# Optimization experiments

Hardware: AMD Instinct MI355X
Metric: run time of the kernel (lower is better)

Reference implementation:

```python
import jax, jax.numpy as jnp
import numpy as np

B, T, HW = 2, 16, 224
S = 14            # patch size after stem: 56 // 4
FEAT = 64 * S * S # 12544 per stream


def _stem(x, w):
    # I3D truncated at MaxPool3d_2a_3x3: Conv3d 7x7x7 stride 2 (+ReLU) then MaxPool (1,3,3) stride (1,2,2)
    y = jax.lax.conv_general_dilated(x, w, window_strides=(2, 2, 2), padding='SAME',
                                     dimension_numbers=('NCDHW', 'OIDHW', 'NCDHW'))
    y = jax.nn.relu(y)
    y = jax.lax.reduce_window(y, -jnp.inf, jax.lax.max,
                              (1, 1, 1, 3, 3), (1, 1, 1, 2, 2), 'SAME')
    return y  # [B,64,8,56,56]


def _fold_and_flatten(x):
    # torch: x.unfold(3,s,s).unfold(4,s,s).permute(0,2,3,4,1,5,6).flatten(4)
    b, c, t, h, w = x.shape
    x = x.reshape(b, c, t, h // S, S, w // S, S)          # (B,C,T,hb,hi,wb,wi)
    x = x.transpose(0, 2, 3, 5, 1, 4, 6)                  # (B,T,hb,wb,C,hi,wi)
    return x.reshape(b, t, h // S, w // S, c * S * S)      # (B,8,4,4,12544)


def _fcl(fr, ff, W1, b1, W2, b2, W3, b3):
    # vectorized over (B,T,H,W); dropout inactive (eval)
    x = jnp.concatenate([fr, ff], axis=-1)                 # (B,8,4,4,25088)
    x = jax.nn.relu(jnp.einsum('bthwf,fk->bthwk', x, W1) + b1)
    x = jax.nn.relu(jnp.einsum('bthwf,fk->bthwk', x, W2) + b2)
    return jax.nn.sigmoid(jnp.einsum('bthwf,fk->bthwk', x, W3) + b3)  # (B,8,4,4,1)


def _get_mask(rgbs, flows, w_rgb, w_flow, W1, b1, W2, b2, W3, b3):
    fr = _fold_and_flatten(_stem(rgbs, w_rgb))
    ff = _fold_and_flatten(_stem(flows, w_flow))
    m = _fcl(fr, ff, W1, b1, W2, b2, W3, b3)[..., 0]       # (B,T=8,H=4,W=4)
    m = jax.image.resize(m[:, None], (m.shape[0], 1, T, HW, HW), method='trilinear')
    return m[:, 0]                                          # (B,16,224,224)


def _masking(rgbs, mask, bg):
    # rgbs*mask + bg*(1-mask), broadcast over channel dim
    return rgbs * mask[:, None] + bg[None, :, None] * (1.0 - mask[:, None])


def _feature_head(x, w_feat, Wl, bl):
    # stand-in for full frozen I3D feature backbone: stem + global pool + linear logits
    y = _stem(x, w_feat)                                    # (B,64,8,56,56)
    pooled = y.mean(axis=(2, 3, 4))                         # (B,64)
    return pooled @ Wl + bl                                 # (B,400)


def setup_inputs() -> dict:
    key = jax.random.key(0)
    ks = jax.random.split(key, 10)
    n = lambda k, s, sc=1.0: jax.random.normal(k, s, dtype=jnp.float32) * sc
    return {
        'rgbs': n(ks[0], (B, 3, T, HW, HW)),
        'flows': n(ks[1], (B, 2, T, HW, HW)),
        'img_background': n(ks[2], (3, HW, HW)),
        'w_rgb': n(ks[3], (64, 3, 7, 7, 7), 0.05),
        'w_flow': n(ks[4], (64, 2, 7, 7, 7), 0.05),
        'w_feat': n(ks[5], (64, 3, 7, 7, 7), 0.05),
        'W1': n(ks[6], (2 * FEAT, 1024), 0.01), 'b1': jnp.zeros((1024,), jnp.float32),
        'W2': n(ks[7], (1024, 256), 0.03), 'b2': jnp.zeros((256,), jnp.float32),
        'W3': n(ks[8], (256, 1), 0.06), 'b3': jnp.zeros((1,), jnp.float32),
        'Wl': n(ks[9], (64, 400), 0.1), 'bl': jnp.zeros((400,), jnp.float32),
    }


def reference(rgbs, flows, img_background, w_rgb, w_flow, w_feat,
              W1, b1, W2, b2, W3, b3, Wl, bl):
    mask = _get_mask(rgbs, flows, w_rgb, w_flow, W1, b1, W2, b2, W3, b3)
    masked0 = _masking(rgbs, mask, img_background)
    masked1 = _masking(rgbs, 1.0 - mask, img_background)
    out0 = _feature_head(masked0, w_feat, Wl, bl)
    out1 = _feature_head(masked1, w_feat, Wl, bl)
    return out0, out1, mask
```

## Files before the change

### kernel.cpp

```cpp
#include <hip/hip_runtime.h>
#include <hip/hip_bf16.h>
#include <math.h>

#define IHW 224
#define DIN 16
#define DOUT 8
#define HO 112
#define PO 56
#define DP 21
#define HP 232
#define WP 240
#define PLANE (HP * WP)

typedef __bf16 bf16x8 __attribute__((ext_vector_type(8)));
typedef float f32x4 __attribute__((ext_vector_type(4)));
typedef float f32x16 __attribute__((ext_vector_type(16)));
typedef ushort u16x8 __attribute__((ext_vector_type(8)));

__device__ __forceinline__ ushort f2bf(float f) {
  uint u = __float_as_uint(f);
  uint r = (u + 0x7FFFu + ((u >> 16) & 1u)) >> 16;
  return (ushort)r;
}
__device__ __forceinline__ float bf2f(ushort u) {
  return __uint_as_float(((uint)u) << 16);
}

__global__ void cvt_pad(const float* __restrict__ in, ushort* __restrict__ out, int nbc) {
  const int v = blockIdx.x * 256 + threadIdx.x;
  const int total = nbc * DP * HP * (WP / 2);
  if (v >= total) return;
  const int pw2 = v % (WP / 2);
  int rest = v / (WP / 2);
  const int pih = rest % HP; rest /= HP;
  const int pid = rest % DP;
  const int bc = rest / DP;
  const int id = pid - 2, ih = pih - 2;
  ushort2 o = make_ushort2(0, 0);
  if (id >= 0 && id < DIN && ih >= 0 && ih < IHW) {
    const float* src = in + ((size_t)(bc * DIN + id) * IHW + ih) * IHW;
    const int iw0 = pw2 * 2 - 2;
    if (iw0 >= 0 && iw0 < IHW) o.x = f2bf(src[iw0]);
    if (iw0 + 1 >= 0 && iw0 + 1 < IHW) o.y = f2bf(src[iw0 + 1]);
  }
  reinterpret_cast<ushort2*>(out)[v] = o;
}

__global__ void masking_pad(const float* __restrict__ rgbs, const float* __restrict__ mask,
                            const float* __restrict__ bg, ushort* __restrict__ out) {
  const int v = blockIdx.x * 256 + threadIdx.x;
  const int total = 12 * DP * HP * (WP / 2);
  if (v >= total) return;
  const int pw2 = v % (WP / 2);
  int rest = v / (WP / 2);
  const int pih = rest % HP; rest /= HP;
  const int pid = rest % DP;
  const int bc = rest / DP;
  const int head = bc / 6;
  const int r6 = bc - head * 6;
  const int b = r6 / 3, c = r6 - (r6 / 3) * 3;
  const int t = pid - 2, ih = pih - 2;
  ushort2 o = make_ushort2(0, 0);
  if (t >= 0 && t < DIN && ih >= 0 && ih < IHW) {
    const float* mrow = mask + ((size_t)(b * DIN + t)) * (IHW * IHW) + ih * IHW;
    const float* rrow = rgbs + ((size_t)((b * 3 + c) * DIN + t)) * (IHW * IHW) + ih * IHW;
    const float* brow = bg + (size_t)c * (IHW * IHW) + ih * IHW;
    const int iw0 = pw2 * 2 - 2;
#pragma unroll
    for (int j = 0; j < 2; j++) {
      const int iw = iw0 + j;
      if (iw >= 0 && iw < IHW) {
        float m = mrow[iw];
        if (head) m = 1.f - m;
        const float val = rrow[iw] * m + brow[iw] * (1.f - m);
        if (j == 0) o.x = f2bf(val); else o.y = f2bf(val);
      }
    }
  }
  reinterpret_cast<ushort2*>(out)[v] = o;
}

template<int C>
__global__ __launch_bounds__(256) void wprep(const float* __restrict__ w, ushort* __restrict__ wB) {
  constexpr int C7 = C * 7, KREAL = C * 49, KPAD = (C == 3) ? 160 : 128;
  const int idx = blockIdx.x * 256 + threadIdx.x;
  if (idx >= 64 * 7 * KPAD) return;
  const int k = idx % KPAD;
  const int rest = idx / KPAD;
  const int kw = rest % 7;
  const int oc = rest / 7;
  float val = 0.f;
  if (k < KREAL) {
    const int kd = k / C7, rem = k % C7, c = rem / 7, kh = rem % 7;
    val = w[(((oc * C + c) * 7 + kd) * 7 + kh) * 7 + kw];
  }
  wB[idx] = f2bf(val);
}

template<int C>
__global__ __launch_bounds__(256, 4) void conv_mfma(
    const ushort* __restrict__ in, const ushort* __restrict__ wB,
    ushort* __restrict__ out)
{
  constexpr int C7 = C * 7, KREAL = C * 49;
  constexpr int KPAD = (C == 3) ? 160 : 128;
  constexpr int NKS = KPAD / 16;
  constexpr int ROWB = KPAD * 2;
  constexpr int KG = KPAD / 4;
  constexpr int SROWS = 118;
  constexpr int NU2 = KG * 64 / 256;
  constexpr int BAT = NU2 / 2;

  __shared__ char smem[SROWS * ROWB];
  __shared__ int offt[KPAD];

  const int bx = blockIdx.x;
  const int hx = (bx & 7) * 28 + (bx >> 3);
  const int ho = hx >> 1, half = hx & 1;
  const int dd = blockIdx.y;
  const int bb = blockIdx.z;
  const int tid = threadIdx.x;
  const int lane = tid & 63;
  const int wv = tid >> 6;

  if (tid < KPAD) {
    const int k = (tid < KREAL) ? tid : (KREAL - 1);
    const int kd = k / C7, rem = k % C7, c = rem / 7, kh = rem % 7;
    offt[tid] = ((bb * C + c) * DP + 2 * dd + kd) * PLANE + (2 * ho + kh) * WP;
  }
  __syncthreads();

  const int piwbase = half * 112;
  for (int itb = 0; itb < 2; itb++) {
    uint v4[BAT][4];
    int sbl[BAT], sbh[BAT];
#pragma unroll
    for (int i = 0; i < BAT; i++) {
      const int id = (itb * BAT + i) * 256 + tid;
      const int kg = id >> 6, sp = id & 63;
      const int s = sp * 2;
      const bool ok = (s < SROWS);
      const int piw = piwbase + s;
      const int4 ot = *reinterpret_cast<const int4*>(&offt[kg * 4]);
      v4[i][0] = *reinterpret_cast<const uint*>(in + (size_t)(ot.x + piw));
      v4[i][1] = *reinterpret_cast<const uint*>(in + (size_t)(ot.y + piw));
      v4[i][2] = *reinterpret_cast<const uint*>(in + (size_t)(ot.z + piw));
      v4[i][3] = *reinterpret_cast<const uint*>(in + (size_t)(ot.w + piw));
      const int m = (sp & 7) << 4;
      sbl[i] = ok ? ((s * ROWB + kg * 8) ^ m) : -1;
      sbh[i] = ok ? (((s + 1) * ROWB + kg * 8) ^ m) : -1;
    }
#pragma unroll
    for (int i = 0; i < BAT; i++) {
      if (sbl[i] >= 0) {
        ushort4 lo, hi;
        lo.x = (ushort)v4[i][0]; hi.x = (ushort)(v4[i][0] >> 16);
        lo.y = (ushort)v4[i][1]; hi.y = (ushort)(v4[i][1] >> 16);
        lo.z = (ushort)v4[i][2]; hi.z = (ushort)(v4[i][2] >> 16);
        lo.w = (ushort)v4[i][3]; hi.w = (ushort)(v4[i][3] >> 16);
        *reinterpret_cast<ushort4*>(smem + sbl[i]) = lo;
        *reinterpret_cast<ushort4*>(smem + sbh[i]) = hi;
      }
    }
  }
  __syncthreads();

  const int nh = wv & 1, kseg = wv >> 1;
  const int l31 = lane & 31, khf = lane >> 5;

  int sbase[2];
#pragma unroll
  for (int mt = 0; mt < 2; mt++) {
    int wo_l = mt * 32 + l31;
    if (wo_l > 55) wo_l = 55;
    sbase[mt] = 2 * wo_l;
  }
  const ushort* wq = wB + (size_t)(nh * 32 + l31) * (7 * KPAD) + khf * 8;

  f32x16 acc[2] = {};

  if (kseg == 0) {
#pragma unroll
    for (int kw = 0; kw < 4; kw++) {
      bf16x8 bq[NKS];
#pragma unroll
      for (int ks = 0; ks < NKS; ks++)
        bq[ks] = *reinterpret_cast<const bf16x8*>(wq + kw * KPAD + ks * 16);
#pragma unroll
      for (int ks = 0; ks < NKS; ks++) {
#pragma unroll
        for (int mt = 0; mt < 2; mt++) {
          const int s = sbase[mt] + kw;
          const int byte = (s * ROWB + ks * 32 + khf * 16) ^ (((s >> 1) & 7) << 4);
          const bf16x8 a = *reinterpret_cast<const bf16x8*>(smem + byte);
          acc[mt] = __builtin_amdgcn_mfma_f32_32x32x16_bf16(a, bq[ks], acc[mt], 0, 0, 0);
        }
      }
    }
  } else {
#pragma unroll
    for (int kw = 4; kw < 7; kw++) {
      bf16x8 bq[NKS];
#pragma unroll
      for (int ks = 0; ks < NKS; ks++)
        bq[ks] = *reinterpret_cast<const bf16x8*>(wq + kw * KPAD + ks * 16);
#pragma unroll
      for (int ks = 0; ks < NKS; ks++) {
#pragma unroll
        for (int mt = 0; mt < 2; mt++) {
          const int s = sbase[mt] + kw;
          const int byte = (s * ROWB + ks * 32 + khf * 16) ^ (((s >> 1) & 7) << 4);
          const bf16x8 a = *reinterpret_cast<const bf16x8*>(smem + byte);
          acc[mt] = __builtin_amdgcn_mfma_f32_32x32x16_bf16(a, bq[ks], acc[mt], 0, 0, 0);
        }
      }
    }
  }

  __syncthreads();
  float* redf = reinterpret_cast<float*>(smem);
  if (kseg == 1) {
#pragma unroll
    for (int mt = 0; mt < 2; mt++)
#pragma unroll
      for (int r = 0; r < 16; r++)
        redf[((nh * 2 + mt) * 16 + r) * 64 + lane] = acc[mt][r];
  }
  __syncthreads();
  if (kseg == 0) {
#pragma unroll
    for (int mt = 0; mt < 2; mt++)
#pragma unroll
      for (int r = 0; r < 16; r++)
        acc[mt][r] += redf[((nh * 2 + mt) * 16 + r) * 64 + lane];
  }
  __syncthreads();

  ushort* eLDS = reinterpret_cast<ushort*>(smem);
  if (kseg == 0) {
    const int oc = nh * 32 + l31;
#pragma unroll
    for (int mt = 0; mt < 2; mt++) {
#pragma unroll
      for (int q = 0; q < 4; q++) {
        const int wo_b = mt * 32 + q * 8 + khf * 4;
        if (wo_b < 56) {
          ushort4 r4;
          r4.x = f2bf(fmaxf(acc[mt][q * 4 + 0], 0.f));
          r4.y = f2bf(fmaxf(acc[mt][q * 4 + 1], 0.f));
          r4.z = f2bf(fmaxf(acc[mt][q * 4 + 2], 0.f));
          r4.w = f2bf(fmaxf(acc[mt][q * 4 + 3], 0.f));
          *reinterpret_cast<ushort4*>(eLDS + oc * 60 + wo_b) = r4;
        }
      }
    }
  }
  __syncthreads();
  ushort* gout = out + ((size_t)(bb * 64) * DOUT + dd) * (HO * HO) + ho * HO + half * 56;
#pragma unroll
  for (int i = 0; i < 4; i++) {
    const int idx = i * 256 + tid;
    if (idx < 896) {
      const int o2 = idx / 14;
      const int w4 = idx - o2 * 14;
      *reinterpret_cast<ushort4*>(gout + (size_t)o2 * DOUT * (HO * HO) + w4 * 4) =
          *reinterpret_cast<const ushort4*>(eLDS + o2 * 60 + w4 * 4);
    }
  }
}

__global__ void maxpool_gather(const ushort* __restrict__ in, ushort* __restrict__ X, int fbase) {
  const int idx = blockIdx.x * 256 + threadIdx.x;
  if (idx >= 2 * 64 * 8 * PO * 28) return;
  const int wo2 = idx % 28;
  const int ho = (idx / 28) % PO;
  const int rest = idx / (28 * PO);
  const ushort* p = in + (size_t)rest * (HO * HO);
  const int iwb = wo2 * 4;
  ushort m0 = 0, m1 = 0;
  for (int dh = 0; dh < 3; dh++) {
    const int ih = 2 * ho + dh;
    if (ih >= HO) break;
    const ushort* row = p + ih * HO;
    const ushort2 u0 = *reinterpret_cast<const ushort2*>(row + iwb);
    const ushort2 u1 = *reinterpret_cast<const ushort2*>(row + iwb + 2);
    const ushort e4 = (iwb + 4 < HO) ? row[iwb + 4] : (ushort)0;
    ushort a = (u0.x > u0.y) ? u0.x : u0.y;  a = (a > u1.x) ? a : u1.x;
    ushort b2 = (u1.x > u1.y) ? u1.x : u1.y; b2 = (b2 > e4) ? b2 : e4;
    m0 = (a > m0) ? a : m0;
    m1 = (b2 > m1) ? b2 : m1;
  }
  const int wo = wo2 * 2;
  const int t = rest % 8;
  const int c = (rest / 8) % 64;
  const int b = rest / 512;
  const int r = ((b * 8 + t) * 4 + ho / 14) * 4 + (wo / 14);
  const int f = fbase + c * 196 + (ho % 14) * 14 + (wo % 14);
  *reinterpret_cast<ushort2*>(X + (size_t)r * 25088 + f) = make_ushort2(m0, m1);
}

__global__ __launch_bounds__(512) void fcl1_mfma(
    const ushort* __restrict__ X, const float* __restrict__ W1, ushort* __restrict__ part)
{
  const int bn = blockIdx.x;
  const int kc = blockIdx.y;
  const int tid = threadIdx.x;
  const int lane = tid & 63;
  const int wv = tid >> 6;
  const int wm = wv >> 1, wn = wv & 1;
  const int l31 = lane & 31, kh = lane >> 5;

  __shared__ char xs[256 * 128];
  __shared__ char wsm[128 * 128];

  f32x16 acc[2][2] = {};

  const int kchunk0 = kc * 256;

  for (int kt = 0; kt < 4; kt++) {
    const int k0 = kchunk0 + kt * 64;
    __syncthreads();
#pragma unroll
    for (int i = 0; i < 4; i++) {
      const int chunk = tid + 512 * i;
      const int r = chunk >> 3, c8 = chunk & 7;
      const int4 v = *reinterpret_cast<const int4*>(X + (size_t)r * 25088 + k0 + c8 * 8);
      int byte = r * 128 + c8 * 16;
      byte ^= ((r & 7) << 4);
      *reinterpret_cast<int4*>(xs + byte) = v;
    }
    {
      const int nq = tid & 31, kp0 = tid >> 5;
#pragma unroll
      for (int h = 0; h < 2; h++) {
        const int kk = (kp0 + h * 16) * 2;
        const float4 a  = *reinterpret_cast<const float4*>(W1 + (size_t)(k0 + kk) * 1024 + bn * 128 + nq * 4);
        const float4 bq = *reinterpret_cast<const float4*>(W1 + (size_t)(k0 + kk + 1) * 1024 + bn * 128 + nq * 4);
        const float av[4] = {a.x, a.y, a.z, a.w};
        const float bv[4] = {bq.x, bq.y, bq.z, bq.w};
#pragma unroll
        for (int j = 0; j < 4; j++) {
          const int n = nq * 4 + j;
          const uint pack = (uint)f2bf(av[j]) | ((uint)f2bf(bv[j]) << 16);
          const int byte = (n * 128 + kk * 2) ^ ((n & 7) << 4);
          *reinterpret_cast<uint*>(wsm + byte) = pack;
        }
      }
    }
    __syncthreads();
#pragma unroll
    for (int ks = 0; ks < 4; ks++) {
      bf16x8 af[2], bfr[2];
#pragma unroll
      for (int m = 0; m < 2; m++) {
        const int r = wm * 64 + m * 32 + l31;
        const int byte = (r * 128 + ks * 32 + kh * 16) ^ ((r & 7) << 4);
        af[m] = *reinterpret_cast<const bf16x8*>(xs + byte);
      }
#pragma unroll
      for (int n = 0; n < 2; n++) {
        const int c = wn * 64 + n * 32 + l31;
        const int byte = (c * 128 + ks * 32 + kh * 16) ^ ((c & 7) << 4);
        bfr[n] = *reinterpret_cast<const bf16x8*>(wsm + byte);
      }
#pragma unroll
      for (int m = 0; m < 2; m++)
#pragma unroll
        for (int n = 0; n < 2; n++)
          acc[m][n] = __builtin_amdgcn_mfma_f32_32x32x16_bf16(af[m], bfr[n], acc[m][n], 0, 0, 0);
    }
  }

  ushort* pout = part + (size_t)kc * (256 * 1024);
#pragma unroll
  for (int m = 0; m < 2; m++)
#pragma unroll
    for (int n = 0; n < 2; n++)
#pragma unroll
      for (int rg = 0; rg < 16; rg++) {
        const int row = wm * 64 + m * 32 + (rg & 3) + 8 * (rg >> 2) + 4 * kh;
        const int col = bn * 128 + wn * 64 + n * 32 + l31;
        pout[(size_t)row * 1024 + col] = f2bf(acc[m][n][rg]);
      }
}

__global__ void h1_reduce(const ushort* __restrict__ part, const float* __restrict__ b1,
                          float* __restrict__ h1) {
  const int v = blockIdx.x * 256 + threadIdx.x;
  if (v >= 32768) return;
  const int r = v >> 7, n8 = v & 127;
  float s[8];
#pragma unroll
  for (int j = 0; j < 8; j++) s[j] = b1[n8 * 8 + j];
  for (int kc = 0; kc < 98; kc++) {
    const u16x8 p = *reinterpret_cast<const u16x8*>(part + (size_t)kc * 262144 + r * 1024 + n8 * 8);
#pragma unroll
    for (int j = 0; j < 8; j++) s[j] += bf2f(p[j]);
  }
#pragma unroll
  for (int j = 0; j < 8; j++) h1[r * 1024 + n8 * 8 + j] = fmaxf(s[j], 0.f);
}

__global__ __launch_bounds__(256) void fcl2_k(const float* __restrict__ h1,
                                              const float* __restrict__ W2,
                                              const float* __restrict__ b2,
                                              float* __restrict__ h2) {
  const int r0 = blockIdx.x * 4;
  const int n = threadIdx.x;
  __shared__ float xr[4][1024];
  for (int i = threadIdx.x; i < 4096; i += 256) xr[i >> 10][i & 1023] = h1[r0 * 1024 + i];
  __syncthreads();
  float acc[4] = {b2[n], b2[n], b2[n], b2[n]};
  for (int k = 0; k < 1024; k++) {
    const float w = W2[k * 256 + n];
#pragma unroll
    for (int r = 0; r < 4; r++) acc[r] += xr[r][k] * w;
  }
#pragma unroll
  for (int r = 0; r < 4; r++) h2[(r0 + r) * 256 + n] = fmaxf(acc[r], 0.f);
}

__global__ void fcl3_k(const float* __restrict__ h2, const float* __restrict__ W3,
                       const float* __restrict__ b3, float* __restrict__ ms) {
  __shared__ float w[256];
  w[threadIdx.x] = W3[threadIdx.x];
  __syncthreads();
  const int r = threadIdx.x;
  float s = b3[0];
  for (int k = 0; k < 256; k++) s += h2[r * 256 + k] * w[k];
  ms[r] = 1.f / (1.f + expf(-s));
}

__global__ void upsample_k(const float* __restrict__ ms, float* __restrict__ mask) {
  const int idx = blockIdx.x * 256 + threadIdx.x;
  if (idx >= 2 * 16 * IHW * IHW) return;
  const int w = idx % IHW;
  const int h = (idx / IHW) % IHW;
  const int t = (idx / (IHW * IHW)) % 16;
  const int b = idx / (16 * IHW * IHW);

  const float tf = t * 0.5f - 0.25f;
  const float hf = (h + 0.5f) * (1.f / 56.f) - 0.5f;
  const float wf = (w + 0.5f) * (1.f / 56.f) - 0.5f;

  int t0 = (int)floorf(tf); const float ft = tf - t0;
  int h0 = (int)floorf(hf); const float fh = hf - h0;
  int w0 = (int)floorf(wf); const float fw = wf - w0;
  const int t1 = min(t0 + 1, 7); t0 = max(t0, 0);
  const int h1 = min(h0 + 1, 3); h0 = max(h0, 0);
  const int w1 = min(w0 + 1, 3); w0 = max(w0, 0);

  const float* p = ms + b * 128;
  auto at = [&](int tt, int hh, int ww) { return p[(tt * 4 + hh) * 4 + ww]; };
  const float c00 = at(t0, h0, w0) * (1.f - fw) + at(t0, h0, w1) * fw;
  const float c01 = at(t0, h1, w0) * (1.f - fw) + at(t0, h1, w1) * fw;
  const float c10 = at(t1, h0, w0) * (1.f - fw) + at(t1, h0, w1) * fw;
  const float c11 = at(t1, h1, w0) * (1.f - fw) + at(t1, h1, w1) * fw;
  const float c0 = c00 * (1.f - fh) + c01 * fh;
  const float c1 = c10 * (1.f - fh) + c11 * fh;
  mask[idx] = c0 * (1.f - ft) + c1 * ft;
}

__global__ __launch_bounds__(256) void pool_sum_k(const ushort* __restrict__ in,
                                                  float* __restrict__ psums) {
  const int blk = blockIdx.x;
  const ushort* p = in + (size_t)blk * (HO * HO);
  float s = 0.f;
  for (int idx = threadIdx.x; idx < PO * PO; idx += 256) {
    const int ho = idx / PO, wo = idx % PO;
    ushort m = 0;
    for (int dh = 0; dh < 3; dh++) {
      const int ih = 2 * ho + dh;
      if (ih >= HO) break;
      for (int dw = 0; dw < 3; dw++) {
        const int iw = 2 * wo + dw;
        if (iw >= HO) break;
        const ushort v = p[ih * HO + iw];
        m = (v > m) ? v : m;
      }
    }
    s += bf2f(m);
  }
  __shared__ float red[256];
  red[threadIdx.x] = s;
  __syncthreads();
  for (int off = 128; off > 0; off >>= 1) {
    if (threadIdx.x < off) red[threadIdx.x] += red[threadIdx.x + off];
    __syncthreads();
  }
  if (threadIdx.x == 0) psums[blk] = red[0];
}

__global__ void logits_k(const float* __restrict__ psums, const float* __restrict__ Wl,
                         const float* __restrict__ bl, float* __restrict__ out) {
  const int idx = blockIdx.x * 256 + threadIdx.x;
  if (idx >= 1600) return;
  const int bf = idx / 400, l = idx % 400;
  float s = bl[l];
  for (int oc = 0; oc < 64; oc++) {
    float ps = 0.f;
    for (int t = 0; t < 8; t++) ps += psums[(bf * 64 + oc) * 8 + t];
    s += (ps * (1.f / 25088.f)) * Wl[oc * 400 + l];
  }
  out[idx] = s;
}

extern "C" void kernel_launch(void* const* d_in, const int* in_sizes, int n_in,
                              void* d_out, int out_size, void* d_ws, size_t ws_size,
                              hipStream_t stream) {
  const float* rgbs   = (const float*)d_in[0];
  const float* flows  = (const float*)d_in[1];
  const float* bg     = (const float*)d_in[2];
  const float* w_rgb  = (const float*)d_in[3];
  const float* w_flow = (const float*)d_in[4];
  const float* w_feat = (const float*)d_in[5];
  const float* W1     = (const float*)d_in[6];
  const float* b1     = (const float*)d_in[7];
  const float* W2     = (const float*)d_in[8];
  const float* b2     = (const float*)d_in[9];
  const float* W3     = (const float*)d_in[10];
  const float* b3     = (const float*)d_in[11];
  const float* Wl     = (const float*)d_in[12];
  const float* bl     = (const float*)d_in[13];
  float* out = (float*)d_out;

  float* ws = (float*)d_ws;
  ushort* convbuf = (ushort*)ws;
  ushort* part    = (ushort*)ws;
  ushort* X       = (ushort*)(ws + 12845056);
  ushort* rgbsP   = (ushort*)(ws + 16056320);
  ushort* flowsP  = (ushort*)(ws + 19564160);
  ushort* maskedP = (ushort*)(ws + 16056320);
  float*  h1      = ws + 23100000;
  float*  h2      = h1 + 262144;
  float*  msmall  = h2 + 65536;
  float*  psums   = msmall + 256;
  ushort* wrgb_b  = (ushort*)(psums + 2048);
  ushort* wflow_b = wrgb_b + 86016;
  ushort* wfeat_b = wflow_b + 57344;

  float* mask_full = out + 1600;

  cvt_pad<<<(3507840 + 255) / 256, 256, 0, stream>>>(rgbs, rgbsP, 6);
  cvt_pad<<<(2338560 + 255) / 256, 256, 0, stream>>>(flows, flowsP, 4);
  wprep<3><<<(64 * 7 * 160 + 255) / 256, 256, 0, stream>>>(w_rgb, wrgb_b);
  wprep<2><<<(64 * 7 * 128 + 255) / 256, 256, 0, stream>>>(w_flow, wflow_b);
  wprep<3><<<(64 * 7 * 160 + 255) / 256, 256, 0, stream>>>(w_feat, wfeat_b);

  conv_mfma<3><<<dim3(224, 8, 2), 256, 0, stream>>>(rgbsP, wrgb_b, convbuf);
  maxpool_gather<<<(1605632 + 255) / 256, 256, 0, stream>>>(convbuf, X, 0);
  conv_mfma<2><<<dim3(224, 8, 2), 256, 0, stream>>>(flowsP, wflow_b, convbuf);
  maxpool_gather<<<(1605632 + 255) / 256, 256, 0, stream>>>(convbuf, X, 12544);

  fcl1_mfma<<<dim3(8, 98), 512, 0, stream>>>(X, W1, part);
  h1_reduce<<<128, 256, 0, stream>>>(part, b1, h1);
  fcl2_k<<<64, 256, 0, stream>>>(h1, W2, b2, h2);
  fcl3_k<<<1, 256, 0, stream>>>(h2, W3, b3, msmall);
  upsample_k<<<(1605632 + 255) / 256, 256, 0, stream>>>(msmall, mask_full);

  masking_pad<<<(7015680 + 255) / 256, 256, 0, stream>>>(rgbs, mask_full, bg, maskedP);
  conv_mfma<3><<<dim3(224, 8, 4), 256, 0, stream>>>(maskedP, wfeat_b, convbuf);
  pool_sum_k<<<2048, 256, 0, stream>>>(convbuf, psums);
  logits_k<<<7, 256, 0, stream>>>(psums, Wl, bl, out);
}
```

Measured before the change: 449.6 us.

## Split conv K-loop across four wave groups with 512-thread blocks

Doubles conv_mfma block size to 512 threads so the seven kernel-width taps are split across four wave groups instead of two. Partial accumulators are combined through a two-level LDS reduction tree, and the staging and store loops are rescaled to the larger block. This shortens each wave's serial MFMA chain and raises wave count, at the cost of extra reduction barriers and uneven tap split. For the 2-channel variant the second reduction buffer may extend past the shared staging array.

```diff
diff --git a/kernel.cpp b/kernel.cpp
--- a/kernel.cpp
+++ b/kernel.cpp
@@ -98,7 +98,7 @@
 }
 
 template<int C>
-__global__ __launch_bounds__(256, 4) void conv_mfma(
+__global__ __launch_bounds__(512, 4) void conv_mfma(
     const ushort* __restrict__ in, const ushort* __restrict__ wB,
     ushort* __restrict__ out)
 {
@@ -108,8 +108,7 @@
   constexpr int ROWB = KPAD * 2;
   constexpr int KG = KPAD / 4;
   constexpr int SROWS = 118;
-  constexpr int NU2 = KG * 64 / 256;
-  constexpr int BAT = NU2 / 2;
+  constexpr int NU2 = KG * 64 / 512;
 
   __shared__ char smem[SROWS * ROWB];
   __shared__ int offt[KPAD];
@@ -130,13 +129,13 @@
   }
   __syncthreads();
 
-  const int piwbase = half * 112;
-  for (int itb = 0; itb < 2; itb++) {
-    uint v4[BAT][4];
-    int sbl[BAT], sbh[BAT];
-#pragma unroll
-    for (int i = 0; i < BAT; i++) {
-      const int id = (itb * BAT + i) * 256 + tid;
+  {
+    const int piwbase = half * 112;
+    uint v4[NU2][4];
+    int sbl[NU2], sbh[NU2];
+#pragma unroll
+    for (int i = 0; i < NU2; i++) {
+      const int id = i * 512 + tid;
       const int kg = id >> 6, sp = id & 63;
       const int s = sp * 2;
       const bool ok = (s < SROWS);
@@ -151,7 +150,7 @@
       sbh[i] = ok ? (((s + 1) * ROWB + kg * 8) ^ m) : -1;
     }
 #pragma unroll
-    for (int i = 0; i < BAT; i++) {
+    for (int i = 0; i < NU2; i++) {
       if (sbl[i] >= 0) {
         ushort4 lo, hi;
         lo.x = (ushort)v4[i][0]; hi.x = (ushort)(v4[i][0] >> 16);
@@ -179,52 +178,61 @@
 
   f32x16 acc[2] = {};
 
+  const int kwbeg = kseg * 2;
+  const int kwend = (kseg == 3) ? 7 : (kwbeg + 2);
+  for (int kw = kwbeg; kw < kwend; kw++) {
+#pragma unroll
+    for (int ks = 0; ks < NKS; ks++) {
+      const bf16x8 b = *reinterpret_cast<const bf16x8*>(wq + kw * KPAD + ks * 16);
+#pragma unroll
+      for (int mt = 0; mt < 2; mt++) {
+        const int s = sbase[mt] + kw;
+        const int byte = (s * ROWB + ks * 32 + khf * 16) ^ (((s >> 1) & 7) << 4);
+        const bf16x8 a = *reinterpret_cast<const bf16x8*>(smem + byte);
+        acc[mt] = __builtin_amdgcn_mfma_f32_32x32x16_bf16(a, b, acc[mt], 0, 0, 0);
+      }
+    }
+  }
+
+  __syncthreads();
+  float* buf0 = reinterpret_cast<float*>(smem);
+  float* buf1 = reinterpret_cast<float*>(smem + 16384);
+  if (kseg == 1) {
+#pragma unroll
+    for (int mt = 0; mt < 2; mt++)
+#pragma unroll
+      for (int r = 0; r < 16; r++)
+        buf0[((nh * 2 + mt) * 16 + r) * 64 + lane] = acc[mt][r];
+  }
+  if (kseg == 3) {
+#pragma unroll
+    for (int mt = 0; mt < 2; mt++)
+#pragma unroll
+      for (int r = 0; r < 16; r++)
+        buf1[((nh * 2 + mt) * 16 + r) * 64 + lane] = acc[mt][r];
+  }
+  __syncthreads();
   if (kseg == 0) {
 #pragma unroll
-    for (int kw = 0; kw < 4; kw++) {
-      bf16x8 bq[NKS];
-#pragma unroll
-      for (int ks = 0; ks < NKS; ks++)
-        bq[ks] = *reinterpret_cast<const bf16x8*>(wq + kw * KPAD + ks * 16);
-#pragma unroll
-      for (int ks = 0; ks < NKS; ks++) {
-#pragma unroll
-        for (int mt = 0; mt < 2; mt++) {
-          const int s = sbase[mt] + kw;
-          const int byte = (s * ROWB + ks * 32 + khf * 16) ^ (((s >> 1) & 7) << 4);
-          const bf16x8 a = *reinterpret_cast<const bf16x8*>(smem + byte);
-          acc[mt] = __builtin_amdgcn_mfma_f32_32x32x16_bf16(a, bq[ks], acc[mt], 0, 0, 0);
-        }
-      }
-    }
-  } else {
-#pragma unroll
-    for (int kw = 4; kw < 7; kw++) {
-      bf16x8 bq[NKS];
-#pragma unroll
-      for (int ks = 0; ks < NKS; ks++)
-        bq[ks] = *reinterpret_cast<const bf16x8*>(wq + kw * KPAD + ks * 16);
-#pragma unroll
-      for (int ks = 0; ks < NKS; ks++) {
-#pragma unroll
-        for (int mt = 0; mt < 2; mt++) {
-          const int s = sbase[mt] + kw;
-          const int byte = (s * ROWB + ks * 32 + khf * 16) ^ (((s >> 1) & 7) << 4);
-          const bf16x8 a = *reinterpret_cast<const bf16x8*>(smem + byte);
-          acc[mt] = __builtin_amdgcn_mfma_f32_32x32x16_bf16(a, bq[ks], acc[mt], 0, 0, 0);
-        }
-      }
-    }
-  }
-
-  __syncthreads();
-  float* redf = reinterpret_cast<float*>(smem);
-  if (kseg == 1) {
-#pragma unroll
     for (int mt = 0; mt < 2; mt++)
 #pragma unroll
       for (int r = 0; r < 16; r++)
-        redf[((nh * 2 + mt) * 16 + r) * 64 + lane] = acc[mt][r];
+        acc[mt][r] += buf0[((nh * 2 + mt) * 16 + r) * 64 + lane];
+  }
+  if (kseg == 2) {
+#pragma unroll
+    for (int mt = 0; mt < 2; mt++)
+#pragma unroll
+      for (int r = 0; r < 16; r++)
+        acc[mt][r] += buf1[((nh * 2 + mt) * 16 + r) * 64 + lane];
+  }
+  __syncthreads();
+  if (kseg == 2) {
+#pragma unroll
+    for (int mt = 0; mt < 2; mt++)
+#pragma unroll
+      for (int r = 0; r < 16; r++)
+        buf0[((nh * 2 + mt) * 16 + r) * 64 + lane] = acc[mt][r];
   }
   __syncthreads();
   if (kseg == 0) {
@@ -232,7 +240,7 @@
     for (int mt = 0; mt < 2; mt++)
 #pragma unroll
       for (int r = 0; r < 16; r++)
-        acc[mt][r] += redf[((nh * 2 + mt) * 16 + r) * 64 + lane];
+        acc[mt][r] += buf0[((nh * 2 + mt) * 16 + r) * 64 + lane];
   }
   __syncthreads();
 
@@ -258,8 +266,8 @@
   __syncthreads();
   ushort* gout = out + ((size_t)(bb * 64) * DOUT + dd) * (HO * HO) + ho * HO + half * 56;
 #pragma unroll
-  for (int i = 0; i < 4; i++) {
-    const int idx = i * 256 + tid;
+  for (int i = 0; i < 2; i++) {
+    const int idx = i * 512 + tid;
     if (idx < 896) {
       const int o2 = idx / 14;
       const int w4 = idx - o2 * 14;
@@ -547,9 +555,9 @@
   wprep<2><<<(64 * 7 * 128 + 255) / 256, 256, 0, stream>>>(w_flow, wflow_b);
   wprep<3><<<(64 * 7 * 160 + 255) / 256, 256, 0, stream>>>(w_feat, wfeat_b);
 
-  conv_mfma<3><<<dim3(224, 8, 2), 256, 0, stream>>>(rgbsP, wrgb_b, convbuf);
+  conv_mfma<3><<<dim3(224, 8, 2), 512, 0, stream>>>(rgbsP, wrgb_b, convbuf);
   maxpool_gather<<<(1605632 + 255) / 256, 256, 0, stream>>>(convbuf, X, 0);
-  conv_mfma<2><<<dim3(224, 8, 2), 256, 0, stream>>>(flowsP, wflow_b, convbuf);
+  conv_mfma<2><<<dim3(224, 8, 2), 512, 0, stream>>>(flowsP, wflow_b, convbuf);
   maxpool_gather<<<(1605632 + 255) / 256, 256, 0, stream>>>(convbuf, X, 12544);
 
   fcl1_mfma<<<dim3(8, 98), 512, 0, stream>>>(X, W1, part);
@@ -559,7 +567,7 @@
   upsample_k<<<(1605632 + 255) / 256, 256, 0, stream>>>(msmall, mask_full);
 
   masking_pad<<<(7015680 + 255) / 256, 256, 0, stream>>>(rgbs, mask_full, bg, maskedP);
-  conv_mfma<3><<<dim3(224, 8, 4), 256, 0, stream>>>(maskedP, wfeat_b, convbuf);
+  conv_mfma<3><<<dim3(224, 8, 4), 512, 0, stream>>>(maskedP, wfeat_b, convbuf);
   pool_sum_k<<<2048, 256, 0, stream>>>(convbuf, psums);
   logits_k<<<7, 256, 0, stream>>>(psums, Wl, bl, out);
 }
```

Result: slower. 508.5 us (+13.1%).
